# Performance work log

Measured on AMD Instinct MI355X. Metric: run time of the kernel, lower is better.

The kernel has to match this reference:

```python
import jax, jax.numpy as jnp
import numpy as np

N_NODES = 100000


def gcn_conv(x, src, dst, ew, W, b, n):
    # PyG GCNConv: x' = D^-1/2 (A + I) D^-1/2 (x W) + b
    h = x @ W  # [N, out]
    deg = jax.ops.segment_sum(ew, dst, num_segments=n)  # weighted in-degree incl self-loops
    dinv = jnp.where(deg > 0, jax.lax.rsqrt(deg), 0.0)
    norm = dinv[src] * ew * dinv[dst]  # [E+N]
    msg = norm[:, None] * h[src]  # gather + scale
    out = jax.ops.segment_sum(msg, dst, num_segments=n)  # scatter-add
    return out + b


def setup_inputs() -> dict:
    key = jax.random.key(0)
    k1, k2, k3, k4, k5 = jax.random.split(key, 5)
    E = 1600000
    x = jax.random.normal(k1, (N_NODES, 128), dtype=jnp.float32)
    edge_index = jax.random.randint(k2, (2, E), 0, N_NODES, dtype=jnp.int64)
    edge_weights = jax.random.uniform(k3, (E,), dtype=jnp.float32)
    W1 = jax.random.normal(k4, (128, 64), dtype=jnp.float32) * (1.0 / np.sqrt(128))
    b1 = jnp.zeros((64,), dtype=jnp.float32)
    W2 = jax.random.normal(k5, (64, 16), dtype=jnp.float32) * (1.0 / np.sqrt(64))
    b2 = jnp.zeros((16,), dtype=jnp.float32)
    return {"x": x, "edge_index": edge_index, "edge_weights": edge_weights,
            "W1": W1, "b1": b1, "W2": W2, "b2": b2}


def reference(x, edge_index, edge_weights, W1, b1, W2, b2):
    n = x.shape[0]
    # add self-loops with weight 1 (PyG gcn_norm default)
    loop = jnp.arange(n, dtype=edge_index.dtype)
    src = jnp.concatenate([edge_index[0], loop])
    dst = jnp.concatenate([edge_index[1], loop])
    ew = jnp.concatenate([edge_weights, jnp.ones((n,), dtype=edge_weights.dtype)])
    h = gcn_conv(x, src, dst, ew, W1, b1, n)
    h = jax.nn.relu(h)
    # dropout: identity in eval mode (F.dropout with training=False)
    h = gcn_conv(h, src, dst, ew, W2, b2, n)
    return jax.nn.log_softmax(h, axis=1)
```

## Files before the change

### kernel.cpp

```cpp
#include <hip/hip_runtime.h>
#include <cstdint>

#define BLK 256
#define ABLK 512
#define BBLK 1024
#define EJ 4
#define CHUNK (BBLK * EJ)
#define SLB 6
#define SLN 64
#define SCAP 1536
#define NSMAX 1600

#define S1   2097152.0f
#define IS1  (1.0f / 2097152.0f)
#define DSC  16777216.0f
#define IDSC (1.0f / 16777216.0f)

__device__ inline unsigned short f2bf(float f) {
  unsigned u = __float_as_uint(f);
  return (unsigned short)((u + 0x7FFF + ((u >> 16) & 1)) >> 16);
}
__device__ inline float bflo(unsigned u) { return __uint_as_float(u << 16); }
__device__ inline float bfhi(unsigned u) { return __uint_as_float(u & 0xFFFF0000u); }

__global__ __launch_bounds__(BLK) void k_zeroC(int* __restrict__ cur, int NS) {
  int s = blockIdx.x * BLK + threadIdx.x;
  if (s < NS) cur[s] = s * SCAP;
}

__global__ __launch_bounds__(BBLK) void k_bucket(const int* __restrict__ src,
                                                 const int* __restrict__ dst,
                                                 const float* __restrict__ ew,
                                                 int* __restrict__ cur,
                                                 int2* __restrict__ bpk,
                                                 int n, int E, int NS) {
  __shared__ int c[NSMAX];
  int tid = threadIdx.x;
  for (int i = tid; i < NS; i += BBLK) c[i] = 0;
  __syncthreads();
  int base = blockIdx.x * CHUNK;
  int dloc[EJ];
#pragma unroll
  for (int j = 0; j < EJ; j++) {
    int idx = base + j * BBLK + tid;
    int d = -1;
    if (idx < E) {
      d = dst[idx];
      if ((unsigned)d >= (unsigned)n) d = -1;
    }
    dloc[j] = d;
    if (d >= 0) atomicAdd(&c[d >> SLB], 1);
  }
  __syncthreads();
  for (int s = tid; s < NS; s += BBLK) {
    int cc = c[s];
    if (cc) c[s] = atomicAdd(&cur[s], cc);
  }
  __syncthreads();
#pragma unroll
  for (int j = 0; j < EJ; j++) {
    int idx = base + j * BBLK + tid;
    int d = dloc[j];
    if (d >= 0) {
      int s = d >> SLB;
      int p = atomicAdd(&c[s], 1);
      p = min(max(p, s * SCAP), (s + 1) * SCAP - 1);
      int packed = ((d & (SLN - 1)) << 20) | (src[idx] & 0xFFFFF);
      bpk[p] = make_int2(packed, __float_as_int(ew[idx]));
    }
  }
}

__global__ __launch_bounds__(BLK) void k_dinv(int2* __restrict__ bpk,
                                              int* __restrict__ cur,
                                              float* __restrict__ dinv, int n) {
  __shared__ int wsum[SLN];
  int s = blockIdx.x, tid = threadIdx.x;
  int node0 = s << SLB;
  int e0 = s * SCAP;
  int cnt = min(cur[s], e0 + SCAP) - e0;
  int cntP = min((cnt + 127) & ~127, SCAP);
  if (tid < SLN) wsum[tid] = 0;
  for (int e = cnt + tid; e < cntP; e += BLK) bpk[e0 + e] = make_int2(0, 0);
  if (tid == 0) cur[s] = e0 + cntP;
  __syncthreads();
  for (int e = e0 + tid; e < e0 + cnt; e += BLK) {
    int2 pk = bpk[e];
    atomicAdd(&wsum[(unsigned)pk.x >> 20],
              __float2int_rn(__int_as_float(pk.y) * DSC));
  }
  __syncthreads();
  if (tid < SLN && node0 + tid < n)
    dinv[node0 + tid] = rsqrtf(1.0f + wsum[tid] * IDSC);
}

__global__ __launch_bounds__(BLK) void k_gemm1(const float* __restrict__ x,
                                               const float* __restrict__ W,
                                               const float* __restrict__ dinv,
                                               unsigned* __restrict__ h1s, int n) {
  __shared__ float Ws[128 * 64];
  __shared__ float xs[16][128];
  int tid = threadIdx.x;
  const float4* W4 = (const float4*)W;
  float4* Ws4 = (float4*)Ws;
#pragma unroll
  for (int i = 0; i < 8; i++) Ws4[tid + i * BLK] = W4[tid + i * BLK];
  int row0 = blockIdx.x * 16;
  int nrows = min(16, n - row0);
  const float4* x4 = (const float4*)(x + (size_t)row0 * 128);
  float4* xs4 = (float4*)xs;
  for (int i = tid; i < nrows * 32; i += BLK) xs4[i] = x4[i];
  __syncthreads();
  int col = tid & 63, rg = tid >> 6;
  float acc0 = 0.f, acc1 = 0.f, acc2 = 0.f, acc3 = 0.f;
#pragma unroll 4
  for (int k = 0; k < 128; k++) {
    float w = Ws[k * 64 + col];
    acc0 += xs[rg][k] * w;
    acc1 += xs[rg + 4][k] * w;
    acc2 += xs[rg + 8][k] * w;
    acc3 += xs[rg + 12][k] * w;
  }
  int r = row0 + rg;
  int rc0 = min(r, n - 1), rc1 = min(r + 4, n - 1),
      rc2 = min(r + 8, n - 1), rc3 = min(r + 12, n - 1);
  float v0 = acc0 * dinv[rc0], v1 = acc1 * dinv[rc1],
        v2 = acc2 * dinv[rc2], v3 = acc3 * dinv[rc3];
  float p0 = __shfl_xor(v0, 1, 64), p1 = __shfl_xor(v1, 1, 64),
        p2 = __shfl_xor(v2, 1, 64), p3 = __shfl_xor(v3, 1, 64);
  if ((col & 1) == 0) {
    int dw = col >> 1;
    unsigned u0 = (unsigned)f2bf(v0) | ((unsigned)f2bf(p0) << 16);
    unsigned u1 = (unsigned)f2bf(v1) | ((unsigned)f2bf(p1) << 16);
    unsigned u2 = (unsigned)f2bf(v2) | ((unsigned)f2bf(p2) << 16);
    unsigned u3 = (unsigned)f2bf(v3) | ((unsigned)f2bf(p3) << 16);
    if (r < n)      h1s[(size_t)r * 32 + dw]        = u0;
    if (r + 4 < n)  h1s[(size_t)(r + 4) * 32 + dw]  = u1;
    if (r + 8 < n)  h1s[(size_t)(r + 8) * 32 + dw]  = u2;
    if (r + 12 < n) h1s[(size_t)(r + 12) * 32 + dw] = u3;
  }
}

#define U1 4
__global__ __launch_bounds__(ABLK) void k_agg1s(const float* __restrict__ dinv,
                                                const int2* __restrict__ bpk,
                                                const int* __restrict__ cur,
                                                const unsigned* __restrict__ h1s,
                                                const float* __restrict__ b1,
                                                const float* __restrict__ W2,
                                                unsigned* __restrict__ h2s, int n) {
  __shared__ int accE[SLN * 33];
  __shared__ int accO[SLN * 33];
  __shared__ float W2s[64 * 16];
  __shared__ float dv[SLN];
  __shared__ float bb[64];
  int tid = threadIdx.x;
  int s = blockIdx.x;
  int node0 = s << SLB;
  int sn = min(SLN, n - node0);
  for (int i = tid; i < SLN * 33; i += ABLK) { accE[i] = 0; accO[i] = 0; }
  for (int i = tid; i < 1024; i += ABLK) W2s[i] = W2[i];
  if (tid < SLN) dv[tid] = (tid < sn) ? dinv[node0 + tid] : 0.f;
  if (tid < 64) bb[tid] = b1[tid];
  int e0 = s * SCAP;
  int cnt = min(cur[s], e0 + SCAP) - e0;
  __syncthreads();

  int w = tid >> 6;
  int g4 = (tid >> 4) & 3;
  int l = tid & 15;
  for (int base = w * 16; base < cnt; base += 128) {
    int2 pk[U1];
#pragma unroll
    for (int u = 0; u < U1; u++) pk[u] = bpk[e0 + base + g4 + 4 * u];
    uint2 gg[U1];
#pragma unroll
    for (int u = 0; u < U1; u++)
      gg[u] = *(const uint2*)(h1s +
               (size_t)(unsigned)(pk[u].x & 0xFFFFF) * 32 + 2 * l);
#pragma unroll
    for (int u = 0; u < U1; u++) {
      int a = (int)((unsigned)pk[u].x >> 20) * 33 + 2 * l;
      float wt = __int_as_float(pk[u].y) * S1;
      atomicAdd(&accE[a],     __float2int_rn(wt * bflo(gg[u].x)));
      atomicAdd(&accO[a],     __float2int_rn(wt * bfhi(gg[u].x)));
      atomicAdd(&accE[a + 1], __float2int_rn(wt * bflo(gg[u].y)));
      atomicAdd(&accO[a + 1], __float2int_rn(wt * bfhi(gg[u].y)));
    }
  }
  __syncthreads();
  for (int i = tid; i < SLN * 64; i += ABLK) {
    int node = i >> 6, k = i & 63;
    if (node < sn) {
      int v = node0 + node;
      unsigned us = h1s[(size_t)v * 32 + (k >> 1)];
      float self = (k & 1) ? bfhi(us) : bflo(us);
      int* pl = (k & 1) ? accO : accE;
      int idx = node * 33 + (k >> 1);
      float a = pl[idx] * IS1;
      pl[idx] = __float_as_int(fmaxf(dv[node] * (a + self) + bb[k], 0.f));
    }
  }
  __syncthreads();
  int j = tid & 15;
  for (int nb = 0; nb < SLN; nb += 32) {
    int node = nb + (tid >> 4);
    float p = 0.f;
#pragma unroll
    for (int k = 0; k < 64; k++) {
      float rv = __int_as_float(((k & 1) ? accO : accE)[node * 33 + (k >> 1)]);
      p += rv * W2s[k * 16 + j];
    }
    p *= dv[node];
    float pp = __shfl_xor(p, 1, 64);
    if (node < sn && (j & 1) == 0)
      h2s[(size_t)(node0 + node) * 8 + (j >> 1)] =
          (unsigned)f2bf(p) | ((unsigned)f2bf(pp) << 16);
  }
}

__global__ __launch_bounds__(ABLK) void k_agg2s(const float* __restrict__ dinv,
                                                const int2* __restrict__ bpk,
                                                const int* __restrict__ cur,
                                                const unsigned* __restrict__ h2s,
                                                const float* __restrict__ b2,
                                                float* __restrict__ out, int n) {
  __shared__ int acc2[SLN * 17];
  int tid = threadIdx.x;
  int s = blockIdx.x;
  int node0 = s << SLB;
  int sn = min(SLN, n - node0);
  for (int i = tid; i < SLN * 17; i += ABLK) acc2[i] = 0;
  int e0 = s * SCAP;
  int cnt = min(cur[s], e0 + SCAP) - e0;
  __syncthreads();

  int w = tid >> 6;
  int eg = (tid >> 2) & 15;
  int m = tid & 3;
  for (int base = w * 16; base < cnt; base += 128) {
    int2 pk = bpk[e0 + base + eg];
    uint2 gg = *(const uint2*)(h2s +
               (size_t)(unsigned)(pk.x & 0xFFFFF) * 8 + 2 * m);
    int a = (int)((unsigned)pk.x >> 20) * 17 + 4 * m;
    float wt = __int_as_float(pk.y) * S1;
    atomicAdd(&acc2[a],     __float2int_rn(wt * bflo(gg.x)));
    atomicAdd(&acc2[a + 1], __float2int_rn(wt * bfhi(gg.x)));
    atomicAdd(&acc2[a + 2], __float2int_rn(wt * bflo(gg.y)));
    atomicAdd(&acc2[a + 3], __float2int_rn(wt * bfhi(gg.y)));
  }
  __syncthreads();
  int f = tid & 15;
  for (int nb = 0; nb < SLN; nb += 32) {
    int node = nb + (tid >> 4);
    bool ok = node < sn;
    int v = node0 + min(node, sn - 1);
    float val = 0.f;
    if (ok) {
      float di = dinv[v];
      unsigned us = h2s[(size_t)v * 8 + (f >> 1)];
      float self = (f & 1) ? bfhi(us) : bflo(us);
      val = di * (acc2[node * 17 + f] * IS1 + self) + b2[f];
    }
    float m2 = val;
    m2 = fmaxf(m2, __shfl_xor(m2, 1, 64));
    m2 = fmaxf(m2, __shfl_xor(m2, 2, 64));
    m2 = fmaxf(m2, __shfl_xor(m2, 4, 64));
    m2 = fmaxf(m2, __shfl_xor(m2, 8, 64));
    float ex = expf(val - m2);
    float ssum = ex;
    ssum += __shfl_xor(ssum, 1, 64);
    ssum += __shfl_xor(ssum, 2, 64);
    ssum += __shfl_xor(ssum, 4, 64);
    ssum += __shfl_xor(ssum, 8, 64);
    if (ok) out[(size_t)v * 16 + f] = val - m2 - logf(ssum);
  }
}

extern "C" void kernel_launch(void* const* d_in, const int* in_sizes, int n_in,
                              void* d_out, int out_size, void* d_ws, size_t ws_size,
                              hipStream_t stream) {
  const float* x  = (const float*)d_in[0];
  const int*   ei = (const int*)d_in[1];
  const float* ew = (const float*)d_in[2];
  const float* W1 = (const float*)d_in[3];
  const float* b1 = (const float*)d_in[4];
  const float* W2 = (const float*)d_in[5];
  const float* b2 = (const float*)d_in[6];
  float* out = (float*)d_out;

  int n = in_sizes[0] / 128;
  int E = in_sizes[2];
  const int* src = ei;
  const int* dst = ei + E;

  int NS = ((n - 1) >> SLB) + 1;
  size_t padE = (size_t)NS * SCAP;

  char* wp = (char*)d_ws;
  auto alloc = [&](size_t bytes) -> char* {
    char* r = wp;
    wp += (bytes + 15) & ~(size_t)15;
    return r;
  };
  int*      cur  = (int*)alloc((size_t)(NS + 4) * 4);
  int2*     bpk  = (int2*)alloc(padE * 8);
  float*    dinv = (float*)alloc((size_t)n * 4);
  unsigned* h1s  = (unsigned*)alloc((size_t)n * 32 * 4);
  unsigned* h2s  = (unsigned*)alloc((size_t)n * 8 * 4);

  int gC = (E + CHUNK - 1) / CHUNK;

  k_zeroC<<<(NS + BLK - 1) / BLK, BLK, 0, stream>>>(cur, NS);
  k_bucket<<<gC, BBLK, 0, stream>>>(src, dst, ew, cur, bpk, n, E, NS);
  k_dinv<<<NS, BLK, 0, stream>>>(bpk, cur, dinv, n);
  k_gemm1<<<(n + 15) / 16, BLK, 0, stream>>>(x, W1, dinv, h1s, n);
  k_agg1s<<<NS, ABLK, 0, stream>>>(dinv, bpk, cur, h1s, b1, W2, h2s, n);
  k_agg2s<<<NS, ABLK, 0, stream>>>(dinv, bpk, cur, h2s, b2, out, n);
}
```

Measured before the change: 244.6 us.

## Compute first-layer GEMM with split-bf16 MFMA instead of scalar FP32 FMAs

Rewrites k_gemm1 to use 16x16x32 bf16 MFMA instructions. Each fp32 operand is split into a high and a low bf16 part, and three MFMAs (hh, lh, hl) recover near-fp32 accuracy. W is pre-split and stored in LDS in fragment layout, x is loaded straight from global memory per lane, and each block now covers 64 rows. The aim is to replace the scalar FMA loop with matrix-core throughput; the costs are conversion overhead and three MFMAs per tile.

New measurement: 221.1 us. 1.11x faster.

```diff
diff --git a/kernel.cpp b/kernel.cpp
--- a/kernel.cpp
+++ b/kernel.cpp
@@ -16,12 +16,23 @@
 #define DSC  16777216.0f
 #define IDSC (1.0f / 16777216.0f)
 
+typedef __attribute__((ext_vector_type(8))) short bf16x8;
+typedef __attribute__((ext_vector_type(4))) float f32x4;
+
 __device__ inline unsigned short f2bf(float f) {
   unsigned u = __float_as_uint(f);
   return (unsigned short)((u + 0x7FFF + ((u >> 16) & 1)) >> 16);
 }
 __device__ inline float bflo(unsigned u) { return __uint_as_float(u << 16); }
 __device__ inline float bfhi(unsigned u) { return __uint_as_float(u & 0xFFFF0000u); }
+
+__device__ inline void splitpk(float a, float b, unsigned& h, unsigned& l) {
+  unsigned short ha = f2bf(a), hb = f2bf(b);
+  h = (unsigned)ha | ((unsigned)hb << 16);
+  float ra = a - __uint_as_float((unsigned)ha << 16);
+  float rb = b - __uint_as_float((unsigned)hb << 16);
+  l = (unsigned)f2bf(ra) | ((unsigned)f2bf(rb) << 16);
+}
 
 __global__ __launch_bounds__(BLK) void k_zeroC(int* __restrict__ cur, int NS) {
   int s = blockIdx.x * BLK + threadIdx.x;
@@ -98,46 +109,66 @@
                                                const float* __restrict__ W,
                                                const float* __restrict__ dinv,
                                                unsigned* __restrict__ h1s, int n) {
-  __shared__ float Ws[128 * 64];
-  __shared__ float xs[16][128];
+  __shared__ unsigned Wh[4][4][64][4];
+  __shared__ unsigned Wl[4][4][64][4];
   int tid = threadIdx.x;
-  const float4* W4 = (const float4*)W;
-  float4* Ws4 = (float4*)Ws;
-#pragma unroll
-  for (int i = 0; i < 8; i++) Ws4[tid + i * BLK] = W4[tid + i * BLK];
-  int row0 = blockIdx.x * 16;
-  int nrows = min(16, n - row0);
-  const float4* x4 = (const float4*)(x + (size_t)row0 * 128);
-  float4* xs4 = (float4*)xs;
-  for (int i = tid; i < nrows * 32; i += BLK) xs4[i] = x4[i];
-  __syncthreads();
-  int col = tid & 63, rg = tid >> 6;
-  float acc0 = 0.f, acc1 = 0.f, acc2 = 0.f, acc3 = 0.f;
-#pragma unroll 4
-  for (int k = 0; k < 128; k++) {
-    float w = Ws[k * 64 + col];
-    acc0 += xs[rg][k] * w;
-    acc1 += xs[rg + 4][k] * w;
-    acc2 += xs[rg + 8][k] * w;
-    acc3 += xs[rg + 12][k] * w;
-  }
-  int r = row0 + rg;
-  int rc0 = min(r, n - 1), rc1 = min(r + 4, n - 1),
-      rc2 = min(r + 8, n - 1), rc3 = min(r + 12, n - 1);
-  float v0 = acc0 * dinv[rc0], v1 = acc1 * dinv[rc1],
-        v2 = acc2 * dinv[rc2], v3 = acc3 * dinv[rc3];
-  float p0 = __shfl_xor(v0, 1, 64), p1 = __shfl_xor(v1, 1, 64),
-        p2 = __shfl_xor(v2, 1, 64), p3 = __shfl_xor(v3, 1, 64);
-  if ((col & 1) == 0) {
-    int dw = col >> 1;
-    unsigned u0 = (unsigned)f2bf(v0) | ((unsigned)f2bf(p0) << 16);
-    unsigned u1 = (unsigned)f2bf(v1) | ((unsigned)f2bf(p1) << 16);
-    unsigned u2 = (unsigned)f2bf(v2) | ((unsigned)f2bf(p2) << 16);
-    unsigned u3 = (unsigned)f2bf(v3) | ((unsigned)f2bf(p3) << 16);
-    if (r < n)      h1s[(size_t)r * 32 + dw]        = u0;
-    if (r + 4 < n)  h1s[(size_t)(r + 4) * 32 + dw]  = u1;
-    if (r + 8 < n)  h1s[(size_t)(r + 8) * 32 + dw]  = u2;
-    if (r + 12 < n) h1s[(size_t)(r + 12) * 32 + dw] = u3;
+  for (int i = tid; i < 4096; i += BLK) {
+    int dw = i & 3, lane = (i >> 2) & 63, ct = (i >> 8) & 3, ks = i >> 10;
+    int col = ct * 16 + (lane & 15);
+    int kb = ks * 32 + ((lane >> 4) << 3) + dw * 2;
+    unsigned h, l;
+    splitpk(W[kb * 64 + col], W[(kb + 1) * 64 + col], h, l);
+    Wh[ks][ct][lane][dw] = h;
+    Wl[ks][ct][lane][dw] = l;
+  }
+  __syncthreads();
+
+  int w = tid >> 6, l = tid & 63;
+  int rowA = blockIdx.x * 64 + w * 16 + (l & 15);
+  int rowAc = min(rowA, n - 1);
+  int kg = l >> 4;
+  const float4* xr = (const float4*)(x + (size_t)rowAc * 128);
+
+  f32x4 acc[4];
+#pragma unroll
+  for (int ct = 0; ct < 4; ct++) acc[ct] = (f32x4){0.f, 0.f, 0.f, 0.f};
+
+  union Frag { unsigned u[4]; bf16x8 s; };
+#pragma unroll
+  for (int ks = 0; ks < 4; ks++) {
+    float4 f0 = xr[ks * 8 + kg * 2];
+    float4 f1 = xr[ks * 8 + kg * 2 + 1];
+    Frag Ah, Al;
+    splitpk(f0.x, f0.y, Ah.u[0], Al.u[0]);
+    splitpk(f0.z, f0.w, Ah.u[1], Al.u[1]);
+    splitpk(f1.x, f1.y, Ah.u[2], Al.u[2]);
+    splitpk(f1.z, f1.w, Ah.u[3], Al.u[3]);
+#pragma unroll
+    for (int ct = 0; ct < 4; ct++) {
+      Frag Bh, Bl;
+      *(uint4*)Bh.u = *(const uint4*)Wh[ks][ct][l];
+      *(uint4*)Bl.u = *(const uint4*)Wl[ks][ct][l];
+      acc[ct] = __builtin_amdgcn_mfma_f32_16x16x32_bf16(Ah.s, Bh.s, acc[ct], 0, 0, 0);
+      acc[ct] = __builtin_amdgcn_mfma_f32_16x16x32_bf16(Al.s, Bh.s, acc[ct], 0, 0, 0);
+      acc[ct] = __builtin_amdgcn_mfma_f32_16x16x32_bf16(Ah.s, Bl.s, acc[ct], 0, 0, 0);
+    }
+  }
+
+  int rbase = blockIdx.x * 64 + w * 16 + (l >> 4) * 4;
+  float di[4];
+#pragma unroll
+  for (int r = 0; r < 4; r++) di[r] = dinv[min(rbase + r, n - 1)];
+  int cl = l & 15;
+#pragma unroll
+  for (int ct = 0; ct < 4; ct++) {
+#pragma unroll
+    for (int r = 0; r < 4; r++) {
+      float v = acc[ct][r] * di[r];
+      float vp = __shfl_xor(v, 1, 64);
+      if ((cl & 1) == 0 && rbase + r < n)
+        h1s[(size_t)(rbase + r) * 32 + ct * 8 + (cl >> 1)] =
+            (unsigned)f2bf(v) | ((unsigned)f2bf(vp) << 16);
+    }
   }
 }
 
@@ -314,7 +345,7 @@
   k_zeroC<<<(NS + BLK - 1) / BLK, BLK, 0, stream>>>(cur, NS);
   k_bucket<<<gC, BBLK, 0, stream>>>(src, dst, ew, cur, bpk, n, E, NS);
   k_dinv<<<NS, BLK, 0, stream>>>(bpk, cur, dinv, n);
-  k_gemm1<<<(n + 15) / 16, BLK, 0, stream>>>(x, W1, dinv, h1s, n);
+  k_gemm1<<<(n + 63) / 64, BLK, 0, stream>>>(x, W1, dinv, h1s, n);
   k_agg1s<<<NS, ABLK, 0, stream>>>(dinv, bpk, cur, h1s, b1, W2, h2s, n);
   k_agg2s<<<NS, ABLK, 0, stream>>>(dinv, bpk, cur, h2s, b2, out, n);
 }
```
